# Optimization experiments

Measured on AMD Instinct MI355X. Metric: run time of the kernel, lower is better.

## Reference

```python
import jax, jax.numpy as jnp
from jax import lax
import numpy as np

B, T, C = 16, 2048, 1024
H, K = 16, 31
R = C // H
P = K - 1  # padding_l (causal)


def setup_inputs() -> dict:
    key = jax.random.key(0)
    kx, kw = jax.random.split(key)
    x = jax.random.normal(kx, (B, T, C), dtype=jnp.float32)
    # kaiming_uniform_(a=sqrt(5)) on (H, 1, K): fan_in = K, bound = 1/sqrt(K)
    bound = 1.0 / np.sqrt(K)
    weight = jax.random.uniform(kw, (H, 1, K), dtype=jnp.float32,
                                minval=-bound, maxval=bound)
    return {"x": x, "weight": weight}


def reference(x, weight):
    # weight_softmax=True: softmax over kernel dim (done in fp32, as in source)
    w = jax.nn.softmax(weight.reshape(H, K).astype(jnp.float32), axis=-1)
    w = w.astype(x.dtype)
    # Each head's kernel is shared across R = C//H channels -> depthwise kernel (C, 1, K)
    w_c = jnp.repeat(w, R, axis=0)            # (C, K)
    kernel = w_c[:, None, :]                  # (C, 1, K) in OIH layout
    x_t = jnp.transpose(x, (0, 2, 1))         # (B, C, T)
    # Cross-correlation with left pad P, right pad K-1-P (same math as the
    # banded-matrix _forward_expanded path / unfold1d + matmul)
    out = lax.conv_general_dilated(
        x_t, kernel,
        window_strides=(1,),
        padding=[(P, K - 1 - P)],
        feature_group_count=C,
        dimension_numbers=("NCH", "OIH", "NCH"),
    )                                         # (B, C, T)
    return jnp.transpose(out, (0, 2, 1))      # (B, T, C)
```

## Files before the change

### kernel.cpp

```cpp
#include <hip/hip_runtime.h>
#include <math.h>

#define TPB 256
#define KW  31
#define TT  16
#define SUB 8
#define BT  (TT * SUB)
constexpr int B_ = 16, T_ = 2048, C_ = 1024, H_ = 16;
constexpr int C2 = C_ / 2;
constexpr int PPH = 32;

__global__ void softmax_rev_kernel(const float* __restrict__ w, float* __restrict__ wr) {
    int h = threadIdx.x;
    if (h < H_) {
        float v[KW];
        float m = -1e30f;
        #pragma unroll
        for (int k = 0; k < KW; ++k) { v[k] = w[h * KW + k]; m = fmaxf(m, v[k]); }
        float s = 0.f;
        #pragma unroll
        for (int k = 0; k < KW; ++k) { v[k] = expf(v[k] - m); s += v[k]; }
        float inv = 1.f / s;
        #pragma unroll
        for (int k = 0; k < KW; ++k) wr[h * KW + (KW - 1 - k)] = v[k] * inv;
    }
}

__global__ __launch_bounds__(TPB, 2) void lconv_kernel(const float2* __restrict__ x,
                                                       const float* __restrict__ wr,
                                                       float2* __restrict__ out) {
    const int h    = blockIdx.x;
    const int pair = threadIdx.x & 31;
    const int sub  = threadIdx.x >> 5;
    const int b    = blockIdx.z;
    const int t0   = blockIdx.y * BT + sub * TT;
    const int c2   = h * PPH + pair;

    float wv[KW];
    #pragma unroll
    for (int j = 0; j < KW; ++j) wv[j] = wr[h * KW + j];

    const float2* px = x   + (size_t)b * T_ * C2 + c2;
    float2*       po = out + (size_t)b * T_ * C2 + c2;

    float2 win[TT + KW - 1];
    if (blockIdx.y == 0 && sub < 2) {
        #pragma unroll
        for (int s = 0; s < TT + KW - 1; ++s) {
            const int t = t0 - (KW - 1) + s;
            win[s] = (t >= 0) ? px[(size_t)t * C2] : make_float2(0.f, 0.f);
        }
    } else {
        #pragma unroll
        for (int s = 0; s < TT + KW - 1; ++s) {
            const int t = t0 - (KW - 1) + s;
            win[s] = px[(size_t)t * C2];
        }
    }

    __builtin_amdgcn_sched_barrier(0);

    #pragma unroll
    for (int i = 0; i < TT; ++i) {
        float ax = 0.f, ay = 0.f;
        #pragma unroll
        for (int j = 0; j < KW; ++j) {
            const float2 v = win[i + KW - 1 - j];
            ax = fmaf(wv[j], v.x, ax);
            ay = fmaf(wv[j], v.y, ay);
        }
        po[(size_t)(t0 + i) * C2] = make_float2(ax, ay);
    }
}

extern "C" void kernel_launch(void* const* d_in, const int* in_sizes, int n_in,
                              void* d_out, int out_size, void* d_ws, size_t ws_size,
                              hipStream_t stream) {
    const float* x = (const float*)d_in[0];
    const float* w = (const float*)d_in[1];
    float* out = (float*)d_out;
    float* wr  = (float*)d_ws;

    hipLaunchKernelGGL(softmax_rev_kernel, dim3(1), dim3(64), 0, stream, w, wr);

    dim3 grid(H_, T_ / BT, B_);
    hipLaunchKernelGGL(lconv_kernel, grid, dim3(TPB), 0, stream,
                       (const float2*)x, wr, (float2*)out);
}
```

Measured before the change: 56.64 us.

## Stage input tile into LDS via global_load_lds and stream-accumulate outputs

Each block now copies its whole time tile plus halo into shared memory with direct global-to-LDS loads, replacing the per-thread register windows that reloaded overlapping halo rows from global memory. The compute loop then reads each row once from LDS and scatters its contribution into sixteen output accumulators. Out-of-range rows are clamped and zeroed in LDS for the first tile. The aim is to cut redundant global traffic from overlapping halos, at the cost of LDS usage, an extra barrier, and dropping the occupancy hint in launch_bounds.

```diff
diff --git a/kernel.cpp b/kernel.cpp
--- a/kernel.cpp
+++ b/kernel.cpp
@@ -1,11 +1,14 @@
 #include <hip/hip_runtime.h>
 #include <math.h>
 
-#define TPB 256
-#define KW  31
-#define TT  16
-#define SUB 8
-#define BT  (TT * SUB)
+#define TPB  256
+#define KW   31
+#define HALO (KW - 1)
+#define TT   16
+#define SUB  8
+#define BT   (TT * SUB)
+#define ROWS (BT + HALO)
+#define RQ   40
 constexpr int B_ = 16, T_ = 2048, C_ = 1024, H_ = 16;
 constexpr int C2 = C_ / 2;
 constexpr int PPH = 32;
@@ -26,51 +29,64 @@
     }
 }
 
-__global__ __launch_bounds__(TPB, 2) void lconv_kernel(const float2* __restrict__ x,
-                                                       const float* __restrict__ wr,
-                                                       float2* __restrict__ out) {
-    const int h    = blockIdx.x;
-    const int pair = threadIdx.x & 31;
-    const int sub  = threadIdx.x >> 5;
-    const int b    = blockIdx.z;
-    const int t0   = blockIdx.y * BT + sub * TT;
-    const int c2   = h * PPH + pair;
+__global__ __launch_bounds__(TPB) void lconv_kernel(const float* __restrict__ x,
+                                                    const float* __restrict__ wr,
+                                                    float* __restrict__ out) {
+    __shared__ float smem[4 * RQ * 64];
+    const int h   = blockIdx.x;
+    const int b   = blockIdx.z;
+    const int t0b = blockIdx.y * BT;
+    const int tid  = threadIdx.x;
+    const int lane = tid & 63;
+    const int wid  = tid >> 6;
+
+    const int qrow  = lane >> 4;
+    const int chunk = lane & 15;
+    const float* xh = x + (size_t)b * T_ * C_ + h * 64;
+    #pragma unroll
+    for (int q = wid; q < RQ; q += 4) {
+        int t = t0b - HALO + 4 * q + qrow;
+        t = min(max(t, 0), T_ - 1);
+        const float* gsrc = xh + (size_t)t * C_ + chunk * 4;
+        __builtin_amdgcn_global_load_lds(
+            (const __attribute__((address_space(1))) uint32_t*)gsrc,
+            (__attribute__((address_space(3))) uint32_t*)(smem + q * 256),
+            16, 0, 0);
+    }
+    __syncthreads();
+    if (blockIdx.y == 0) {
+        for (int k = tid; k < HALO * 64; k += TPB) smem[k] = 0.f;
+        __syncthreads();
+    }
+
+    const int pair = tid & 31;
+    const int sub  = tid >> 5;
 
     float wv[KW];
     #pragma unroll
     for (int j = 0; j < KW; ++j) wv[j] = wr[h * KW + j];
 
-    const float2* px = x   + (size_t)b * T_ * C2 + c2;
-    float2*       po = out + (size_t)b * T_ * C2 + c2;
+    float2 acc[TT];
+    #pragma unroll
+    for (int i = 0; i < TT; ++i) acc[i] = make_float2(0.f, 0.f);
 
-    float2 win[TT + KW - 1];
-    if (blockIdx.y == 0 && sub < 2) {
+    const float2* sm2 = (const float2*)smem;
+    #pragma unroll
+    for (int sr = 0; sr < TT + HALO; ++sr) {
+        const float2 v = sm2[(size_t)(sub * TT + sr) * PPH + pair];
+        const int ilo = (sr - HALO < 0) ? 0 : sr - HALO;
+        const int ihi = (sr < TT - 1) ? sr : TT - 1;
         #pragma unroll
-        for (int s = 0; s < TT + KW - 1; ++s) {
-            const int t = t0 - (KW - 1) + s;
-            win[s] = (t >= 0) ? px[(size_t)t * C2] : make_float2(0.f, 0.f);
-        }
-    } else {
-        #pragma unroll
-        for (int s = 0; s < TT + KW - 1; ++s) {
-            const int t = t0 - (KW - 1) + s;
-            win[s] = px[(size_t)t * C2];
+        for (int i = ilo; i <= ihi; ++i) {
+            const float wj = wv[i + HALO - sr];
+            acc[i].x = fmaf(wj, v.x, acc[i].x);
+            acc[i].y = fmaf(wj, v.y, acc[i].y);
         }
     }
 
-    __builtin_amdgcn_sched_barrier(0);
-
+    float2* po = (float2*)out + ((size_t)b * T_ + t0b + sub * TT) * C2 + h * PPH + pair;
     #pragma unroll
-    for (int i = 0; i < TT; ++i) {
-        float ax = 0.f, ay = 0.f;
-        #pragma unroll
-        for (int j = 0; j < KW; ++j) {
-            const float2 v = win[i + KW - 1 - j];
-            ax = fmaf(wv[j], v.x, ax);
-            ay = fmaf(wv[j], v.y, ay);
-        }
-        po[(size_t)(t0 + i) * C2] = make_float2(ax, ay);
-    }
+    for (int i = 0; i < TT; ++i) po[(size_t)i * C2] = acc[i];
 }
 
 extern "C" void kernel_launch(void* const* d_in, const int* in_sizes, int n_in,
@@ -84,6 +100,5 @@
     hipLaunchKernelGGL(softmax_rev_kernel, dim3(1), dim3(64), 0, stream, w, wr);
 
     dim3 grid(H_, T_ / BT, B_);
-    hipLaunchKernelGGL(lconv_kernel, grid, dim3(TPB), 0, stream,
-                       (const float2*)x, wr, (float2*)out);
+    hipLaunchKernelGGL(lconv_kernel, grid, dim3(TPB), 0, stream, x, wr, out);
 }
```

Result: faster. 50.67 us (-10.5%).
